# Kernel optimization log

Measured on AMD Instinct MI355X. Metric: run time of the kernel, lower is better.

## Reference

```python
import jax, jax.numpy as jnp
import numpy as np

MODEL_DIM = 1024
NUM_HEADS = 16
HEAD_DIM = MODEL_DIM // NUM_HEADS


def setup_inputs() -> dict:
    key = jax.random.key(0)
    ks = jax.random.split(key, 9)
    B, S, D = 2, 2048, MODEL_DIM
    scale = 1.0 / np.sqrt(D)
    X = jax.random.normal(ks[0], (B, S, D), dtype=jnp.float32)
    Wq = jax.random.normal(ks[1], (D, D), dtype=jnp.float32) * scale
    bq = jax.random.normal(ks[2], (D,), dtype=jnp.float32) * 0.01
    Wk = jax.random.normal(ks[3], (D, D), dtype=jnp.float32) * scale
    bk = jax.random.normal(ks[4], (D,), dtype=jnp.float32) * 0.01
    Wv = jax.random.normal(ks[5], (D, D), dtype=jnp.float32) * scale
    bv = jax.random.normal(ks[6], (D,), dtype=jnp.float32) * 0.01
    Wo = jax.random.normal(ks[7], (D, D), dtype=jnp.float32) * scale
    bo = jax.random.normal(ks[8], (D,), dtype=jnp.float32) * 0.01
    return {"X": X, "Wq": Wq, "bq": bq, "Wk": Wk, "bk": bk,
            "Wv": Wv, "bv": bv, "Wo": Wo, "bo": bo}


def reference(X, Wq, bq, Wk, bk, Wv, bv, Wo, bo):
    B, S, D = X.shape
    H, Hd = NUM_HEADS, HEAD_DIM
    # QKV projections (torch Linear: x @ W.T + b; here W stored as (in, out))
    q = (X @ Wq + bq).reshape(B, S, H, Hd)
    k = (X @ Wk + bk).reshape(B, S, H, Hd)
    v = (X @ Wv + bv).reshape(B, S, H, Hd)
    # scores [B, H, S, S]
    score = jnp.einsum('bqhd,bkhd->bhqk', q, k) / jnp.sqrt(jnp.float32(Hd))
    causal = jnp.tril(jnp.ones((S, S), dtype=bool))
    score = jnp.where(causal[None, None], score, -jnp.inf)
    attn = jax.nn.softmax(score, axis=-1)
    out = jnp.einsum('bhqk,bkhd->bqhd', attn, v).reshape(B, S, D)
    return out @ Wo + bo
```

## Files before the change

### kernel.cpp

```cpp
#include <hip/hip_runtime.h>
#include <hip/hip_bf16.h>


#define D_MODEL 1024
#define SEQ     2048
#define NHEADS  16
#define HDIM    64
#define MROWS   4096
#define QSCALE  0.18033688011112042f

typedef __attribute__((ext_vector_type(8))) short short8;
typedef __attribute__((ext_vector_type(8))) _Float16 h8;
typedef __attribute__((ext_vector_type(4))) _Float16 h4;
typedef __attribute__((ext_vector_type(2))) __fp16 fp16x2;
typedef __attribute__((ext_vector_type(4))) float f32x4;

__device__ __forceinline__ ushort f2h(float x) {
    union { _Float16 h; ushort u; } c; c.h = (_Float16)x; return c.u;
}

__device__ __forceinline__ float ex2(float x) {
    float r;
    asm("v_exp_f32 %0, %1" : "=v"(r) : "v"(x));
    return r;
}

__device__ __forceinline__ h4 pack4(float p0, float p1, float p2, float p3) {
    union { fp16x2 h[2]; h4 v; } u;
    u.h[0] = __builtin_amdgcn_cvt_pkrtz(p0, p1);
    u.h[1] = __builtin_amdgcn_cvt_pkrtz(p2, p3);
    return u.v;
}

__device__ __forceinline__ unsigned pack2u(float p0, float p1) {
    union { fp16x2 h; unsigned u; } w;
    w.h = __builtin_amdgcn_cvt_pkrtz(p0, p1);
    return w.u;
}

#define GLDS(gp, lp) \
    __builtin_amdgcn_global_load_lds( \
        (const __attribute__((address_space(1))) void*)(gp), \
        (__attribute__((address_space(3))) void*)(lp), 16, 0, 0)

__device__ __forceinline__ const h8* lds_chunk(const ushort* base, int r, int c) {
    return (const h8*)(base + (((r << 3) + (c ^ (r & 7))) << 3));
}

__global__ __launch_bounds__(256) void cvt_x(const float* __restrict__ src,
                                             ushort* __restrict__ dst) {
    int i = blockIdx.x * 256 + threadIdx.x;
    float4 f0 = ((const float4*)src)[i * 2];
    float4 f1 = ((const float4*)src)[i * 2 + 1];
    short8 o;
    o[0] = f2h(f0.x); o[1] = f2h(f0.y); o[2] = f2h(f0.z); o[3] = f2h(f0.w);
    o[4] = f2h(f1.x); o[5] = f2h(f1.y); o[6] = f2h(f1.z); o[7] = f2h(f1.w);
    ((short8*)dst)[i] = o;
}

__global__ __launch_bounds__(256) void cvt_w_t(
    const float* __restrict__ W0, const float* __restrict__ W1,
    const float* __restrict__ W2, const float* __restrict__ W3,
    ushort* __restrict__ Wt) {
    __shared__ ushort Ts[64][72];
    const int tid = threadIdx.x;
    const int n0 = blockIdx.x * 64, k0 = blockIdx.y * 64, z = blockIdx.z;
    const float* W = z == 0 ? W0 : (z == 1 ? W1 : (z == 2 ? W2 : W3));
    #pragma unroll
    for (int i = 0; i < 4; ++i) {
        int t = tid + 256 * i;
        int r = t >> 4, cg = t & 15;
        float4 f = *(const float4*)(W + (size_t)(k0 + r) * D_MODEL + n0 + cg * 4);
        Ts[cg * 4 + 0][r] = f2h(f.x);
        Ts[cg * 4 + 1][r] = f2h(f.y);
        Ts[cg * 4 + 2][r] = f2h(f.z);
        Ts[cg * 4 + 3][r] = f2h(f.w);
    }
    __syncthreads();
    #pragma unroll
    for (int i = 0; i < 2; ++i) {
        int t = tid + 256 * i;
        int nr = t >> 3, kg = t & 7;
        short8 v = *(const short8*)&Ts[nr][kg * 8];
        *(short8*)(Wt + ((size_t)z * D_MODEL + n0 + nr) * D_MODEL + k0 + kg * 8) = v;
    }
}

__device__ __forceinline__ void gemm_mainloop(
    const ushort* __restrict__ A, const ushort* __restrict__ Bt,
    ushort* Xs, ushort* Ws, int m0, int n0, int tid, f32x4 acc[4][4]) {
    const int wave = tid >> 6, lane = tid & 63;
    const int l16 = lane & 15, quad = lane >> 4;
    const int wm = wave >> 1, wn = wave & 1;

    for (int k0 = 0; k0 < D_MODEL; k0 += 64) {
        #pragma unroll
        for (int i = 0; i < 4; ++i) {
            int slot = i * 256 + tid;
            int row = slot >> 3, cs = slot & 7;
            int c = cs ^ (row & 7);
            GLDS(A + (size_t)(m0 + row) * D_MODEL + k0 + c * 8,
                 Xs + (((i << 8) + (wave << 6)) << 3));
        }
        #pragma unroll
        for (int i = 0; i < 4; ++i) {
            int slot = i * 256 + tid;
            int row = slot >> 3, cs = slot & 7;
            int c = cs ^ (row & 7);
            GLDS(Bt + (size_t)(n0 + row) * D_MODEL + k0 + c * 8,
                 Ws + (((i << 8) + (wave << 6)) << 3));
        }
        __syncthreads();
        #pragma unroll
        for (int kk = 0; kk < 2; ++kk) {
            h8 a[4], b[4];
            #pragma unroll
            for (int t = 0; t < 4; ++t) {
                a[t] = *lds_chunk(Xs, wm * 64 + t * 16 + l16, kk * 4 + quad);
                b[t] = *lds_chunk(Ws, wn * 64 + t * 16 + l16, kk * 4 + quad);
            }
            #pragma unroll
            for (int mt = 0; mt < 4; ++mt)
                #pragma unroll
                for (int nt = 0; nt < 4; ++nt)
                    acc[mt][nt] = __builtin_amdgcn_mfma_f32_16x16x32_f16(
                        a[mt], b[nt], acc[mt][nt], 0, 0, 0);
        }
        __syncthreads();
    }
}

__global__ __launch_bounds__(256) void qkv_gemm_h(
    const ushort* __restrict__ Xh, const ushort* __restrict__ Wt,
    const float* __restrict__ bq, const float* __restrict__ bk,
    const float* __restrict__ bv,
    ushort* __restrict__ Qh, ushort* __restrict__ Kh, ushort* __restrict__ Vh) {
    __shared__ ushort Xs[128 * 64];
    __shared__ ushort Ws[128 * 64];
    const int tid = threadIdx.x;
    const int id = blockIdx.x;
    const int xcd = id & 7, t = id >> 3;
    const int bm = (xcd & 3) * 8 + (t & 7);
    const int bn = (xcd >> 2) * 12 + (t >> 3);
    const int m0 = bm * 128, n0 = bn * 128;

    f32x4 acc[4][4];
    #pragma unroll
    for (int mt = 0; mt < 4; ++mt)
        #pragma unroll
        for (int nt = 0; nt < 4; ++nt) acc[mt][nt] = (f32x4){0.f, 0.f, 0.f, 0.f};

    gemm_mainloop(Xh, Wt, Xs, Ws, m0, n0, tid, acc);

    const int wave = tid >> 6, lane = tid & 63;
    const int l16 = lane & 15, quad = lane >> 4;
    const int wm = wave >> 1, wn = wave & 1;
    const int seg = n0 >> 10;
    const float* bias = seg == 0 ? bq : (seg == 1 ? bk : bv);
    ushort* dst = seg == 0 ? Qh : (seg == 1 ? Kh : Vh);
    const float sc = seg == 0 ? QSCALE : 1.0f;

    #pragma unroll
    for (int mt = 0; mt < 4; ++mt)
        #pragma unroll
        for (int r = 0; r < 4; ++r) {
            int m = m0 + wm * 64 + mt * 16 + quad * 4 + r;
            int bi = m >> 11, s = m & 2047;
            #pragma unroll
            for (int nt = 0; nt < 4; ++nt) {
                int n = n0 + wn * 64 + nt * 16 + l16;
                int nn = n & 1023;
                int h = nn >> 6, d = nn & 63;
                float v = (acc[mt][nt][r] + bias[nn]) * sc;
                dst[((size_t)(bi * NHEADS + h) * SEQ + s) * HDIM + d] = f2h(v);
            }
        }
}

__global__ __launch_bounds__(256) void out_gemm_h(
    const ushort* __restrict__ Ah, const ushort* __restrict__ Wot,
    const float* __restrict__ bo, float* __restrict__ Out) {
    __shared__ ushort Xs[128 * 64];
    __shared__ ushort Ws2[64 * 64];
    const int tid = threadIdx.x;
    const int id = blockIdx.x;
    const int xcd = id & 7, t = id >> 3;
    const int bm = (xcd & 3) * 8 + (t & 7);
    const int bn = (xcd >> 2) * 8 + (t >> 3);
    const int m0 = bm * 128, n0 = bn * 64;
    const int wave = tid >> 6, lane = tid & 63;
    const int l16 = lane & 15, quad = lane >> 4;

    f32x4 acc[2][4];
    #pragma unroll
    for (int mt = 0; mt < 2; ++mt)
        #pragma unroll
        for (int nt = 0; nt < 4; ++nt) acc[mt][nt] = (f32x4){0.f, 0.f, 0.f, 0.f};

    for (int k0 = 0; k0 < D_MODEL; k0 += 64) {
        #pragma unroll
        for (int i = 0; i < 4; ++i) {
            int slot = i * 256 + tid;
            int row = slot >> 3, cs = slot & 7;
            int c = cs ^ (row & 7);
            GLDS(Ah + (size_t)(m0 + row) * D_MODEL + k0 + c * 8,
                 Xs + (((i << 8) + (wave << 6)) << 3));
        }
        #pragma unroll
        for (int i = 0; i < 2; ++i) {
            int slot = i * 256 + tid;
            int row = slot >> 3, cs = slot & 7;
            int c = cs ^ (row & 7);
            GLDS(Wot + (size_t)(n0 + row) * D_MODEL + k0 + c * 8,
                 Ws2 + (((i << 8) + (wave << 6)) << 3));
        }
        __syncthreads();
        #pragma unroll
        for (int kk = 0; kk < 2; ++kk) {
            h8 a[2], b[4];
            #pragma unroll
            for (int mt = 0; mt < 2; ++mt)
                a[mt] = *lds_chunk(Xs, wave * 32 + mt * 16 + l16, kk * 4 + quad);
            #pragma unroll
            for (int nt = 0; nt < 4; ++nt)
                b[nt] = *lds_chunk(Ws2, nt * 16 + l16, kk * 4 + quad);
            #pragma unroll
            for (int mt = 0; mt < 2; ++mt)
                #pragma unroll
                for (int nt = 0; nt < 4; ++nt)
                    acc[mt][nt] = __builtin_amdgcn_mfma_f32_16x16x32_f16(
                        a[mt], b[nt], acc[mt][nt], 0, 0, 0);
        }
        __syncthreads();
    }

    #pragma unroll
    for (int mt = 0; mt < 2; ++mt)
        #pragma unroll
        for (int r = 0; r < 4; ++r) {
            int m = m0 + wave * 32 + mt * 16 + quad * 4 + r;
            #pragma unroll
            for (int nt = 0; nt < 4; ++nt) {
                int n = n0 + nt * 16 + l16;
                Out[(size_t)m * D_MODEL + n] = acc[mt][nt][r] + bo[n];
            }
        }
}

__device__ __forceinline__ void attn_step(
    const h8 kf[4][2], const h4 vf[4][4], const h8* qfg,
    f32x4* oacc, float& l_r,
    int kt, int qtg, int qrow, int quad) {
    f32x4 s[4];
    #pragma unroll
    for (int nt = 0; nt < 4; ++nt) {
        f32x4 z = (f32x4){0.f, 0.f, 0.f, 0.f};
        z = __builtin_amdgcn_mfma_f32_16x16x32_f16(kf[nt][0], qfg[0], z, 0, 0, 0);
        z = __builtin_amdgcn_mfma_f32_16x16x32_f16(kf[nt][1], qfg[1], z, 0, 0, 0);
        s[nt] = z;
    }
    if (kt == qtg) {
        #pragma unroll
        for (int nt = 0; nt < 4; ++nt)
            #pragma unroll
            for (int r = 0; r < 4; ++r) {
                int key = kt * 64 + nt * 16 + quad * 4 + r;
                if (key > qrow) s[nt][r] = -1e30f;
            }
    }
    float pn[4];
    h4 pf[4];
    #pragma unroll
    for (int nt = 0; nt < 4; ++nt) {
        float p0 = ex2(s[nt][0] - 8.f);
        float p1 = ex2(s[nt][1] - 8.f);
        float p2 = ex2(s[nt][2] - 8.f);
        float p3 = ex2(s[nt][3] - 8.f);
        pn[nt] = (p0 + p1) + (p2 + p3);
        pf[nt] = pack4(p0, p1, p2, p3);
    }
    l_r += (pn[0] + pn[1]) + (pn[2] + pn[3]);

    #pragma unroll
    for (int dt = 0; dt < 4; ++dt)
        #pragma unroll
        for (int nt = 0; nt < 4; ++nt)
            oacc[dt] = __builtin_amdgcn_mfma_f32_16x16x16f16(
                vf[dt][nt], pf[nt], oacc[dt], 0, 0, 0);
}

__global__ __launch_bounds__(512, 4) void flash_attn_mfma(
    const ushort* __restrict__ Q, const ushort* __restrict__ K,
    const ushort* __restrict__ V, ushort* __restrict__ O) {
    __shared__ ushort Ks[2][64 * 64];
    __shared__ ushort Vt[2][64][72];
    __shared__ ushort Os[8][16][72];

    const int tid  = threadIdx.x;
    const int wave = tid >> 6;
    const int lane = tid & 63;
    const int l16  = lane & 15;
    const int quad = lane >> 4;
    const int wg   = wave & 3;
    const bool heavy = wave < 4;
    const int bh   = blockIdx.y;
    const int b    = bh >> 4, h = bh & 15;
    const int qt0  = blockIdx.x;
    const int qt1  = 31 - qt0;
    const int myqt = heavy ? qt1 : qt0;

    const ushort* Qb = Q + (size_t)bh * SEQ * HDIM;
    const ushort* Kb = K + (size_t)bh * SEQ * HDIM;
    const ushort* Vb = V + (size_t)bh * SEQ * HDIM;

    const int qrow = myqt * 64 + wg * 16 + l16;

    h8 qf[2];
    qf[0] = *(const h8*)(Qb + (size_t)qrow * HDIM + quad * 8);
    qf[1] = *(const h8*)(Qb + (size_t)qrow * HDIM + 32 + quad * 8);

    f32x4 oacc[4];
    #pragma unroll
    for (int dt = 0; dt < 4; ++dt) oacc[dt] = (f32x4){0.f, 0.f, 0.f, 0.f};
    float l_r = 0.f;

    const int vkp = tid & 31, vdg = (tid >> 5) & 7;
    uint4 va, vb4;

    if (heavy) {
        #pragma unroll
        for (int i = 0; i < 2; ++i) {
            int slot = i * 256 + tid;
            int row = slot >> 3, cs = slot & 7;
            int c = cs ^ (row & 7);
            GLDS(Kb + row * HDIM + c * 8,
                 &Ks[0][0] + (((i << 8) + (wave << 6)) << 3));
        }
    } else {
        const ushort* vap = Vb + (size_t)(2 * vkp) * HDIM + vdg * 8;
        va  = *(const uint4*)vap;
        vb4 = *(const uint4*)(vap + HDIM);
    }

    for (int kt = 0; kt <= qt1; ++kt) {
        const int cur = kt & 1;
        if (!heavy) {
            unsigned av[4] = {va.x, va.y, va.z, va.w};
            unsigned bv[4] = {vb4.x, vb4.y, vb4.z, vb4.w};
            #pragma unroll
            for (int j = 0; j < 4; ++j) {
                unsigned lo = (av[j] & 0xffffu) | (bv[j] << 16);
                unsigned hi = (av[j] >> 16) | (bv[j] & 0xffff0000u);
                ((unsigned*)&Vt[cur][vdg * 8 + 2 * j][0])[vkp] = lo;
                ((unsigned*)&Vt[cur][vdg * 8 + 2 * j + 1][0])[vkp] = hi;
            }
        }
        __syncthreads();

        if (kt < qt1) {
            if (heavy) {
                const ushort* Ktile = Kb + (size_t)(kt + 1) * 64 * HDIM;
                #pragma unroll
                for (int i = 0; i < 2; ++i) {
                    int slot = i * 256 + tid;
                    int row = slot >> 3, cs = slot & 7;
                    int c = cs ^ (row & 7);
                    GLDS(Ktile + row * HDIM + c * 8,
                         &Ks[1 - cur][0] + (((i << 8) + (wave << 6)) << 3));
                }
            } else {
                const ushort* vap =
                    Vb + (size_t)((kt + 1) * 64 + 2 * vkp) * HDIM + vdg * 8;
                va  = *(const uint4*)vap;
                vb4 = *(const uint4*)(vap + HDIM);
            }
        }

        if (heavy || kt <= qt0) {
            h8 kf[4][2];
            #pragma unroll
            for (int nt = 0; nt < 4; ++nt) {
                kf[nt][0] = *lds_chunk(&Ks[cur][0], nt * 16 + l16, quad);
                kf[nt][1] = *lds_chunk(&Ks[cur][0], nt * 16 + l16, 4 + quad);
            }
            h4 vf[4][4];
            #pragma unroll
            for (int dt = 0; dt < 4; ++dt)
                #pragma unroll
                for (int nt = 0; nt < 4; ++nt)
                    vf[dt][nt] =
                        *(const h4*)&Vt[cur][dt * 16 + l16][nt * 16 + quad * 4];

            attn_step(kf, vf, qf, oacc, l_r, kt, myqt, qrow, quad);
        }
    }

    {
        float l = l_r;
        l += __shfl_xor(l, 16);
        l += __shfl_xor(l, 32);
        float inv = 1.f / l;
        #pragma unroll
        for (int dt = 0; dt < 4; ++dt)
            #pragma unroll
            for (int r = 0; r < 4; r += 2) {
                unsigned w = pack2u(oacc[dt][r] * inv, oacc[dt][r + 1] * inv);
                *(unsigned*)&Os[wave][l16][dt * 16 + quad * 4 + r] = w;
            }
        asm volatile("s_waitcnt lgkmcnt(0)" ::: "memory");
        int qr = lane >> 2, dc = lane & 3;
        const ushort* src = &Os[wave][qr][dc * 16];
        short8 v0 = *(const short8*)src;
        short8 v1 = *(const short8*)(src + 8);
        int q = myqt * 64 + wg * 16 + qr;
        ushort* orow = O + (((size_t)b * SEQ + q) * NHEADS + h) * HDIM + dc * 16;
        *(short8*)orow = v0;
        *(short8*)(orow + 8) = v1;
    }
}

extern "C" void kernel_launch(void* const* d_in, const int* in_sizes, int n_in,
                              void* d_out, int out_size, void* d_ws, size_t ws_size,
                              hipStream_t stream)
{
    const float* X  = (const float*)d_in[0];
    const float* Wq = (const float*)d_in[1];
    const float* bq = (const float*)d_in[2];
    const float* Wk = (const float*)d_in[3];
    const float* bk = (const float*)d_in[4];
    const float* Wv = (const float*)d_in[5];
    const float* bv = (const float*)d_in[6];
    const float* Wo = (const float*)d_in[7];
    const float* bo = (const float*)d_in[8];
    float* out = (float*)d_out;

    const size_t MAT = (size_t)MROWS * D_MODEL;
    ushort* Xh = (ushort*)d_ws;
    ushort* Wt = Xh + MAT;
    ushort* Qh = Wt + (size_t)4 * D_MODEL * D_MODEL;
    ushort* Kh = Qh + MAT;
    ushort* Vh = Kh + MAT;
    ushort* Ah = Vh + MAT;

    cvt_x<<<dim3(MAT / 8 / 256), 256, 0, stream>>>(X, Xh);
    cvt_w_t<<<dim3(16, 16, 4), 256, 0, stream>>>(Wq, Wk, Wv, Wo, Wt);
    qkv_gemm_h<<<dim3(768), 256, 0, stream>>>(Xh, Wt, bq, bk, bv, Qh, Kh, Vh);
    flash_attn_mfma<<<dim3(16, 2 * NHEADS), 512, 0, stream>>>(Qh, Kh, Vh, Ah);
    out_gemm_h<<<dim3(512), 256, 0, stream>>>(
        Ah, Wt + (size_t)3 * D_MODEL * D_MODEL, bo, out);
}
```

Baseline: 189.3 us.

## Merge conversion kernels, hoist GEMM load addresses, vectorize epilogue stores via swapped MFMA

Folds the X fp16 conversion into the weight-transpose kernel as a fifth z-slice, removing one launch. The GEMM mainloops precompute global and LDS pointers once and advance them per k-step instead of recomputing addresses each iteration. The MFMA operands are swapped so each lane holds four consecutive output columns, which lets the QKV and output epilogues use vector bias loads and packed 8-byte and 16-byte stores instead of scalar ones. The prep kernel gains branch divergence by z, and its X slice does eight loads per thread.

New measurement: 187.8 us. About the same (-0.8%).

```diff
diff --git a/kernel.cpp b/kernel.cpp
--- a/kernel.cpp
+++ b/kernel.cpp
@@ -47,42 +47,47 @@
     return (const h8*)(base + (((r << 3) + (c ^ (r & 7))) << 3));
 }
 
-__global__ __launch_bounds__(256) void cvt_x(const float* __restrict__ src,
-                                             ushort* __restrict__ dst) {
-    int i = blockIdx.x * 256 + threadIdx.x;
-    float4 f0 = ((const float4*)src)[i * 2];
-    float4 f1 = ((const float4*)src)[i * 2 + 1];
-    short8 o;
-    o[0] = f2h(f0.x); o[1] = f2h(f0.y); o[2] = f2h(f0.z); o[3] = f2h(f0.w);
-    o[4] = f2h(f1.x); o[5] = f2h(f1.y); o[6] = f2h(f1.z); o[7] = f2h(f1.w);
-    ((short8*)dst)[i] = o;
-}
-
-__global__ __launch_bounds__(256) void cvt_w_t(
+__global__ __launch_bounds__(256) void prep(
     const float* __restrict__ W0, const float* __restrict__ W1,
     const float* __restrict__ W2, const float* __restrict__ W3,
-    ushort* __restrict__ Wt) {
-    __shared__ ushort Ts[64][72];
+    const float* __restrict__ X,
+    ushort* __restrict__ Wt, ushort* __restrict__ Xh) {
     const int tid = threadIdx.x;
-    const int n0 = blockIdx.x * 64, k0 = blockIdx.y * 64, z = blockIdx.z;
-    const float* W = z == 0 ? W0 : (z == 1 ? W1 : (z == 2 ? W2 : W3));
-    #pragma unroll
-    for (int i = 0; i < 4; ++i) {
-        int t = tid + 256 * i;
-        int r = t >> 4, cg = t & 15;
-        float4 f = *(const float4*)(W + (size_t)(k0 + r) * D_MODEL + n0 + cg * 4);
-        Ts[cg * 4 + 0][r] = f2h(f.x);
-        Ts[cg * 4 + 1][r] = f2h(f.y);
-        Ts[cg * 4 + 2][r] = f2h(f.z);
-        Ts[cg * 4 + 3][r] = f2h(f.w);
-    }
-    __syncthreads();
-    #pragma unroll
-    for (int i = 0; i < 2; ++i) {
-        int t = tid + 256 * i;
-        int nr = t >> 3, kg = t & 7;
-        short8 v = *(const short8*)&Ts[nr][kg * 8];
-        *(short8*)(Wt + ((size_t)z * D_MODEL + n0 + nr) * D_MODEL + k0 + kg * 8) = v;
+    const int z = blockIdx.z;
+    if (z < 4) {
+        __shared__ ushort Ts[64][72];
+        const int n0 = blockIdx.x * 64, k0 = blockIdx.y * 64;
+        const float* W = z == 0 ? W0 : (z == 1 ? W1 : (z == 2 ? W2 : W3));
+        #pragma unroll
+        for (int i = 0; i < 4; ++i) {
+            int t = tid + 256 * i;
+            int r = t >> 4, cg = t & 15;
+            float4 f = *(const float4*)(W + (size_t)(k0 + r) * D_MODEL + n0 + cg * 4);
+            Ts[cg * 4 + 0][r] = f2h(f.x);
+            Ts[cg * 4 + 1][r] = f2h(f.y);
+            Ts[cg * 4 + 2][r] = f2h(f.z);
+            Ts[cg * 4 + 3][r] = f2h(f.w);
+        }
+        __syncthreads();
+        #pragma unroll
+        for (int i = 0; i < 2; ++i) {
+            int t = tid + 256 * i;
+            int nr = t >> 3, kg = t & 7;
+            short8 v = *(const short8*)&Ts[nr][kg * 8];
+            *(short8*)(Wt + ((size_t)z * D_MODEL + n0 + nr) * D_MODEL + k0 + kg * 8) = v;
+        }
+    } else {
+        int base = (blockIdx.y * 16 + blockIdx.x) * 2048 + tid;
+        #pragma unroll
+        for (int i = 0; i < 8; ++i) {
+            int idx = base + i * 256;
+            float4 f0 = ((const float4*)X)[idx * 2];
+            float4 f1 = ((const float4*)X)[idx * 2 + 1];
+            short8 o;
+            o[0] = f2h(f0.x); o[1] = f2h(f0.y); o[2] = f2h(f0.z); o[3] = f2h(f0.w);
+            o[4] = f2h(f1.x); o[5] = f2h(f1.y); o[6] = f2h(f1.z); o[7] = f2h(f1.w);
+            ((short8*)Xh)[idx] = o;
+        }
     }
 }
 
@@ -93,23 +98,23 @@
     const int l16 = lane & 15, quad = lane >> 4;
     const int wm = wave >> 1, wn = wave & 1;
 
+    const ushort* ag[4]; const ushort* bg[4]; ushort* al[4]; ushort* bl[4];
+    #pragma unroll
+    for (int i = 0; i < 4; ++i) {
+        int slot = i * 256 + tid;
+        int row = slot >> 3, cs = slot & 7;
+        int c = cs ^ (row & 7);
+        ag[i] = A + (size_t)(m0 + row) * D_MODEL + c * 8;
+        bg[i] = Bt + (size_t)(n0 + row) * D_MODEL + c * 8;
+        al[i] = Xs + (((i << 8) + (wave << 6)) << 3);
+        bl[i] = Ws + (((i << 8) + (wave << 6)) << 3);
+    }
+
     for (int k0 = 0; k0 < D_MODEL; k0 += 64) {
         #pragma unroll
-        for (int i = 0; i < 4; ++i) {
-            int slot = i * 256 + tid;
-            int row = slot >> 3, cs = slot & 7;
-            int c = cs ^ (row & 7);
-            GLDS(A + (size_t)(m0 + row) * D_MODEL + k0 + c * 8,
-                 Xs + (((i << 8) + (wave << 6)) << 3));
-        }
-        #pragma unroll
-        for (int i = 0; i < 4; ++i) {
-            int slot = i * 256 + tid;
-            int row = slot >> 3, cs = slot & 7;
-            int c = cs ^ (row & 7);
-            GLDS(Bt + (size_t)(n0 + row) * D_MODEL + k0 + c * 8,
-                 Ws + (((i << 8) + (wave << 6)) << 3));
-        }
+        for (int i = 0; i < 4; ++i) { GLDS(ag[i], al[i]); ag[i] += 64; }
+        #pragma unroll
+        for (int i = 0; i < 4; ++i) { GLDS(bg[i], bl[i]); bg[i] += 64; }
         __syncthreads();
         #pragma unroll
         for (int kk = 0; kk < 2; ++kk) {
@@ -124,7 +129,7 @@
                 #pragma unroll
                 for (int nt = 0; nt < 4; ++nt)
                     acc[mt][nt] = __builtin_amdgcn_mfma_f32_16x16x32_f16(
-                        a[mt], b[nt], acc[mt][nt], 0, 0, 0);
+                        b[nt], a[mt], acc[mt][nt], 0, 0, 0);
         }
         __syncthreads();
     }
@@ -161,20 +166,21 @@
     const float sc = seg == 0 ? QSCALE : 1.0f;
 
     #pragma unroll
-    for (int mt = 0; mt < 4; ++mt)
-        #pragma unroll
-        for (int r = 0; r < 4; ++r) {
-            int m = m0 + wm * 64 + mt * 16 + quad * 4 + r;
-            int bi = m >> 11, s = m & 2047;
-            #pragma unroll
-            for (int nt = 0; nt < 4; ++nt) {
-                int n = n0 + wn * 64 + nt * 16 + l16;
-                int nn = n & 1023;
-                int h = nn >> 6, d = nn & 63;
-                float v = (acc[mt][nt][r] + bias[nn]) * sc;
-                dst[((size_t)(bi * NHEADS + h) * SEQ + s) * HDIM + d] = f2h(v);
-            }
-        }
+    for (int mt = 0; mt < 4; ++mt) {
+        int m = m0 + wm * 64 + mt * 16 + l16;
+        int bi = m >> 11, s = m & 2047;
+        #pragma unroll
+        for (int nt = 0; nt < 4; ++nt) {
+            int nn = (n0 + wn * 64 + nt * 16 + quad * 4) & 1023;
+            int h = nn >> 6, d = nn & 63;
+            float4 bb = *(const float4*)(bias + nn);
+            f32x4 v = acc[mt][nt];
+            uint2 w;
+            w.x = pack2u((v[0] + bb.x) * sc, (v[1] + bb.y) * sc);
+            w.y = pack2u((v[2] + bb.z) * sc, (v[3] + bb.w) * sc);
+            *(uint2*)(dst + ((size_t)(bi * NHEADS + h) * SEQ + s) * HDIM + d) = w;
+        }
+    }
 }
 
 __global__ __launch_bounds__(256) void out_gemm_h(
@@ -197,23 +203,29 @@
         #pragma unroll
         for (int nt = 0; nt < 4; ++nt) acc[mt][nt] = (f32x4){0.f, 0.f, 0.f, 0.f};
 
+    const ushort* ag[4]; const ushort* bg[2]; ushort* al[4]; ushort* bl[2];
+    #pragma unroll
+    for (int i = 0; i < 4; ++i) {
+        int slot = i * 256 + tid;
+        int row = slot >> 3, cs = slot & 7;
+        int c = cs ^ (row & 7);
+        ag[i] = Ah + (size_t)(m0 + row) * D_MODEL + c * 8;
+        al[i] = Xs + (((i << 8) + (wave << 6)) << 3);
+    }
+    #pragma unroll
+    for (int i = 0; i < 2; ++i) {
+        int slot = i * 256 + tid;
+        int row = slot >> 3, cs = slot & 7;
+        int c = cs ^ (row & 7);
+        bg[i] = Wot + (size_t)(n0 + row) * D_MODEL + c * 8;
+        bl[i] = Ws2 + (((i << 8) + (wave << 6)) << 3);
+    }
+
     for (int k0 = 0; k0 < D_MODEL; k0 += 64) {
         #pragma unroll
-        for (int i = 0; i < 4; ++i) {
-            int slot = i * 256 + tid;
-            int row = slot >> 3, cs = slot & 7;
-            int c = cs ^ (row & 7);
-            GLDS(Ah + (size_t)(m0 + row) * D_MODEL + k0 + c * 8,
-                 Xs + (((i << 8) + (wave << 6)) << 3));
-        }
-        #pragma unroll
-        for (int i = 0; i < 2; ++i) {
-            int slot = i * 256 + tid;
-            int row = slot >> 3, cs = slot & 7;
-            int c = cs ^ (row & 7);
-            GLDS(Wot + (size_t)(n0 + row) * D_MODEL + k0 + c * 8,
-                 Ws2 + (((i << 8) + (wave << 6)) << 3));
-        }
+        for (int i = 0; i < 4; ++i) { GLDS(ag[i], al[i]); ag[i] += 64; }
+        #pragma unroll
+        for (int i = 0; i < 2; ++i) { GLDS(bg[i], bl[i]); bg[i] += 64; }
         __syncthreads();
         #pragma unroll
         for (int kk = 0; kk < 2; ++kk) {
@@ -229,22 +241,25 @@
                 #pragma unroll
                 for (int nt = 0; nt < 4; ++nt)
                     acc[mt][nt] = __builtin_amdgcn_mfma_f32_16x16x32_f16(
-                        a[mt], b[nt], acc[mt][nt], 0, 0, 0);
-        }
-        __syncthreads();
-    }
-
-    #pragma unroll
-    for (int mt = 0; mt < 2; ++mt)
-        #pragma unroll
-        for (int r = 0; r < 4; ++r) {
-            int m = m0 + wave * 32 + mt * 16 + quad * 4 + r;
-            #pragma unroll
-            for (int nt = 0; nt < 4; ++nt) {
-                int n = n0 + nt * 16 + l16;
-                Out[(size_t)m * D_MODEL + n] = acc[mt][nt][r] + bo[n];
-            }
-        }
+                        b[nt], a[mt], acc[mt][nt], 0, 0, 0);
+        }
+        __syncthreads();
+    }
+
+    #pragma unroll
+    for (int mt = 0; mt < 2; ++mt) {
+        int m = m0 + wave * 32 + mt * 16 + l16;
+        #pragma unroll
+        for (int nt = 0; nt < 4; ++nt) {
+            int n = n0 + nt * 16 + quad * 4;
+            float4 bb = *(const float4*)(bo + n);
+            f32x4 v = acc[mt][nt];
+            float4 o;
+            o.x = v[0] + bb.x; o.y = v[1] + bb.y;
+            o.z = v[2] + bb.z; o.w = v[3] + bb.w;
+            *(float4*)(Out + (size_t)m * D_MODEL + n) = o;
+        }
+    }
 }
 
 __device__ __forceinline__ void attn_step(
@@ -442,8 +457,7 @@
     ushort* Vh = Kh + MAT;
     ushort* Ah = Vh + MAT;
 
-    cvt_x<<<dim3(MAT / 8 / 256), 256, 0, stream>>>(X, Xh);
-    cvt_w_t<<<dim3(16, 16, 4), 256, 0, stream>>>(Wq, Wk, Wv, Wo, Wt);
+    prep<<<dim3(16, 16, 5), 256, 0, stream>>>(Wq, Wk, Wv, Wo, X, Wt, Xh);
     qkv_gemm_h<<<dim3(768), 256, 0, stream>>>(Xh, Wt, bq, bk, bv, Qh, Kh, Vh);
     flash_attn_mfma<<<dim3(16, 2 * NHEADS), 512, 0, stream>>>(Qh, Kh, Vh, Ah);
     out_gemm_h<<<dim3(512), 256, 0, stream>>>(
```
